# Optimization experiments

Measured on AMD Instinct MI355X. Metric: run time of the kernel, lower is better.

Reference implementation:

```python
import jax, jax.numpy as jnp
import numpy as np

B, LQ, LKV = 2, 2048, 2048
DQ, DKV, HID, NH = 1024, 1024, 1024, 16
HD = HID // NH
EPS = 1e-5


def setup_inputs() -> dict:
    key = jax.random.key(0)
    ks = jax.random.split(key, 12)
    s_q = 1.0 / np.sqrt(DQ)
    s_kv = 1.0 / np.sqrt(DKV)
    s_h = 1.0 / np.sqrt(HID)
    return {
        "query": jax.random.normal(ks[0], (B, LQ, DQ), jnp.float32),
        "key_value": jax.random.normal(ks[1], (B, LKV, DKV), jnp.float32),
        "Wq": jax.random.uniform(ks[2], (DQ, HID), jnp.float32, -s_q, s_q),
        "bq": jax.random.uniform(ks[3], (HID,), jnp.float32, -s_q, s_q),
        "Wk": jax.random.uniform(ks[4], (DKV, HID), jnp.float32, -s_kv, s_kv),
        "bk": jax.random.uniform(ks[5], (HID,), jnp.float32, -s_kv, s_kv),
        "Wv": jax.random.uniform(ks[6], (DKV, HID), jnp.float32, -s_kv, s_kv),
        "bv": jax.random.uniform(ks[7], (HID,), jnp.float32, -s_kv, s_kv),
        "Wo": jax.random.uniform(ks[8], (HID, DQ), jnp.float32, -s_h, s_h),
        "bo": jax.random.uniform(ks[9], (DQ,), jnp.float32, -s_h, s_h),
        "ln_gamma": jnp.ones((DQ,), jnp.float32),
        "ln_beta": jnp.zeros((DQ,), jnp.float32),
    }


def reference(query, key_value, Wq, bq, Wk, bk, Wv, bv, Wo, bo, ln_gamma, ln_beta):
    b, lq, _ = query.shape
    lkv = key_value.shape[1]
    # projections -> [b, heads, len, head_dim]
    Q = (query @ Wq + bq).reshape(b, lq, NH, HD).transpose(0, 2, 1, 3)
    K = (key_value @ Wk + bk).reshape(b, lkv, NH, HD).transpose(0, 2, 1, 3)
    V = (key_value @ Wv + bv).reshape(b, lkv, NH, HD).transpose(0, 2, 1, 3)
    scores = jnp.einsum("bhqd,bhkd->bhqk", Q, K) / jnp.sqrt(jnp.float32(HD))
    attn = jax.nn.softmax(scores, axis=-1)
    ctx = jnp.einsum("bhqk,bhkd->bhqd", attn, V)
    ctx = ctx.transpose(0, 2, 1, 3).reshape(b, lq, HID)
    out = ctx @ Wo + bo
    x = query + out
    mu = jnp.mean(x, axis=-1, keepdims=True)
    var = jnp.mean(jnp.square(x - mu), axis=-1, keepdims=True)
    return (x - mu) / jnp.sqrt(var + EPS) * ln_gamma + ln_beta
```

## Files before the change

kernel.cpp:

```cpp
#include <hip/hip_runtime.h>

typedef unsigned short u16;
typedef __bf16 bf16x8 __attribute__((ext_vector_type(8)));
typedef float f32x4 __attribute__((ext_vector_type(4)));
typedef unsigned short u16x4 __attribute__((ext_vector_type(4)));

#define LOG2E 1.44269504088896340736f
#define LDK 1040
#define LDV 2080
#define EXPM16 12599160.0f

__device__ __forceinline__ u16 f2bf(float f) {
  unsigned u = __float_as_uint(f);
  u += 0x7FFFu + ((u >> 16) & 1u);
  return (u16)(u >> 16);
}

__device__ __forceinline__ void load_lds16(const void* g, void* l) {
  __builtin_amdgcn_global_load_lds(
      (__attribute__((address_space(1))) void*)g,
      (__attribute__((address_space(3))) void*)l, 16, 0, 0);
}

__device__ __forceinline__ f32x4 mfma16(bf16x8 a, bf16x8 b, f32x4 c) {
  return __builtin_amdgcn_mfma_f32_16x16x32_bf16(a, b, c, 0, 0, 0);
}

__global__ __launch_bounds__(256) void pre_kernel(
    const float* __restrict__ q, const float* __restrict__ kv,
    u16* __restrict__ Xq, u16* __restrict__ Xkv,
    const float* __restrict__ Wq, const float* __restrict__ Wk,
    const float* __restrict__ Wv, const float* __restrict__ Wo,
    u16* __restrict__ Wqt, u16* __restrict__ Wkt,
    u16* __restrict__ Wvt, u16* __restrict__ Wot) {
  __shared__ float tile[32][33];
  const int bid = blockIdx.x;
  if (bid < 8192) {
    const int n4each = 4096 * 256;
    int i = bid * 256 + threadIdx.x;
    const float* src; u16* dst; int j;
    if (i < n4each) { src = q; dst = Xq; j = i; }
    else            { src = kv; dst = Xkv; j = i - n4each; }
    const float4 v = ((const float4*)src)[j];
    u16x4 o;
    o.x = f2bf(v.x); o.y = f2bf(v.y); o.z = f2bf(v.z); o.w = f2bf(v.w);
    ((u16x4*)dst)[j] = o;
    return;
  }
  const int t = bid - 8192;
  const int z = t >> 10, rem = t & 1023;
  const float* W; u16* Wt;
  switch (z) {
    case 0: W = Wq; Wt = Wqt; break;
    case 1: W = Wk; Wt = Wkt; break;
    case 2: W = Wv; Wt = Wvt; break;
    default: W = Wo; Wt = Wot; break;
  }
  const int tx = threadIdx.x & 31, ty = threadIdx.x >> 5;
  const int n0 = (rem & 31) * 32, k0 = (rem >> 5) * 32;
#pragma unroll
  for (int i = 0; i < 4; i++)
    tile[ty + i * 8][tx] = W[(size_t)(k0 + ty + i * 8) * 1024 + n0 + tx];
  __syncthreads();
#pragma unroll
  for (int i = 0; i < 4; i++)
    Wt[(size_t)(n0 + ty + i * 8) * 1024 + k0 + tx] = f2bf(tile[tx][ty + i * 8]);
}

__device__ __forceinline__ void gemm_tile(
    const u16* __restrict__ A, int lda, const u16* __restrict__ Bt, int ldb,
    const float* __restrict__ bias, bool brow, float scale,
    u16* __restrict__ Cb, float* __restrict__ Cf,
    int ldc, int bm, int bn, int K) {
  __shared__ alignas(16) u16 As[128 * 32];
  __shared__ alignas(16) u16 Bs[128 * 32];
  const int tid = threadIdx.x;
  const int wave = tid >> 6, lane = tid & 63;
  const int lm = lane & 15, kq = lane >> 4;
  const int g1 = tid, g2 = tid + 256;
  const u16* Ag1 = A + (size_t)(bm + (g1 >> 2)) * lda + (g1 & 3) * 8;
  const u16* Ag2 = A + (size_t)(bm + (g2 >> 2)) * lda + (g2 & 3) * 8;
  const u16* Bg1 = Bt + (size_t)(bn + (g1 >> 2)) * ldb + (g1 & 3) * 8;
  const u16* Bg2 = Bt + (size_t)(bn + (g2 >> 2)) * ldb + (g2 & 3) * 8;
  u16* lA1 = &As[g1 * 8]; u16* lA2 = &As[g2 * 8];
  u16* lB1 = &Bs[g1 * 8]; u16* lB2 = &Bs[g2 * 8];
  const int wm = (wave >> 1) * 64, wn = (wave & 1) * 64;

  f32x4 acc[4][4] = {};
  for (int k0 = 0; k0 < K; k0 += 32) {
    __syncthreads();
    load_lds16(Ag1 + k0, lA1);
    load_lds16(Ag2 + k0, lA2);
    load_lds16(Bg1 + k0, lB1);
    load_lds16(Bg2 + k0, lB2);
    __syncthreads();
    bf16x8 a[4], b[4];
#pragma unroll
    for (int t = 0; t < 4; t++)
      a[t] = *(const bf16x8*)&As[(wm + t * 16 + lm) * 32 + kq * 8];
#pragma unroll
    for (int t = 0; t < 4; t++)
      b[t] = *(const bf16x8*)&Bs[(wn + t * 16 + lm) * 32 + kq * 8];
#pragma unroll
    for (int mt = 0; mt < 4; mt++)
#pragma unroll
      for (int nt = 0; nt < 4; nt++)
        acc[mt][nt] = mfma16(a[mt], b[nt], acc[mt][nt]);
  }
#pragma unroll
  for (int mt = 0; mt < 4; mt++) {
    float rb[4];
#pragma unroll
    for (int r = 0; r < 4; r++)
      rb[r] = (bias && brow) ? bias[bm + wm + mt * 16 + kq * 4 + r] : 0.f;
#pragma unroll
    for (int nt = 0; nt < 4; nt++) {
      const int col = bn + wn + nt * 16 + lm;
      const float cb = (bias && !brow) ? bias[col] : 0.f;
#pragma unroll
      for (int r = 0; r < 4; r++) {
        const int row = bm + wm + mt * 16 + kq * 4 + r;
        const size_t idx = (size_t)row * ldc + col;
        const float v = (acc[mt][nt][r] + rb[r] + cb) * scale;
        if (Cf) Cf[idx] = v;
        else    Cb[idx] = f2bf(v);
      }
    }
  }
}

__global__ __launch_bounds__(256) void proj_gemm_kernel(
    const u16* __restrict__ Xq, const u16* __restrict__ Xkv,
    const u16* __restrict__ Wqt, const u16* __restrict__ Wkt, const u16* __restrict__ Wvt,
    const float* __restrict__ bq, const float* __restrict__ bk, const float* __restrict__ bv,
    u16* __restrict__ Qp, u16* __restrict__ Kp, u16* __restrict__ Vt, float qscale) {
  const int bid = blockIdx.x;
  const u16 *A, *Bt; const float* bias; u16* C;
  bool brow = false; float sc = 1.f; int ldc = 1024; int bm, bn;
  if (bid < 512) {
    const int r = bid & 255;
    const int xcd = r & 7, s = r >> 3;
    bm = (xcd * 4 + (s >> 3)) * 128;
    bn = (s & 7) * 128;
    if (bid < 256) { A = Xq;  Bt = Wqt; bias = bq; C = Qp; sc = qscale; }
    else           { A = Xkv; Bt = Wkt; bias = bk; C = Kp; ldc = LDK;  }
  } else {
    int r = bid - 512;
    const int z = r >> 7; r &= 127;
    const int xcd = r & 7, s = r >> 3;
    bm = (s >> 1) * 128;
    bn = (xcd * 2 + (s & 1)) * 128;
    A = Wvt; Bt = Xkv + (size_t)z * 2048 * 1024; bias = bv; brow = true;
    C = Vt + (size_t)z * 1024 * LDV; ldc = LDV;
  }
  gemm_tile(A, 1024, Bt, 1024, bias, brow, sc, C, nullptr, ldc, bm, bn, 1024);
}

__global__ __launch_bounds__(256) void ogemm_kernel(
    const u16* __restrict__ Ctx, const u16* __restrict__ Wot,
    float* __restrict__ X0, float* __restrict__ X1) {
  const int z = blockIdx.z;
  float* Cf = z ? X1 : X0;
  const int lin = blockIdx.x + 8 * blockIdx.y;
  const int xcd = lin & 7, s = lin >> 3;
  const int bm = (xcd * 4 + (s >> 3)) * 128, bn = (s & 7) * 128;
  gemm_tile(Ctx + z * 512, 1024, Wot + z * 512, 1024, nullptr, false, 1.f,
            nullptr, Cf, 1024, bm, bn, 512);
}

__global__ __launch_bounds__(256) void attn_kernel(
    const u16* __restrict__ Qp, const u16* __restrict__ Kp,
    const u16* __restrict__ Vt, u16* __restrict__ ctx) {
  __shared__ alignas(16) u16 Ks[2 * 4096];
  __shared__ alignas(16) u16 Vs[2 * 4096];
  const int tid = threadIdx.x;
  const int wave = tid >> 6, lane = tid & 63;
  const int lm = lane & 15, kq = lane >> 4;
  const int L = blockIdx.x;
  const int xcd = L & 7, s = L >> 3;
  const int combo = xcd + 8 * (s >> 4);
  const int qb = s & 15;
  const int h = combo & 15, b = combo >> 4;
  const int qbase = qb * 128 + wave * 32;

  bf16x8 qf[2][2];
#pragma unroll
  for (int qt = 0; qt < 2; qt++)
#pragma unroll
    for (int kc = 0; kc < 2; kc++)
      qf[qt][kc] = *(const bf16x8*)(Qp + (size_t)(b * 2048 + qbase + qt * 16 + lm) * 1024 +
                                    h * 64 + kc * 32 + kq * 8);

  union { u16 u[8]; bf16x8 v; } uo;
#pragma unroll
  for (int i = 0; i < 8; i++) uo.u[i] = 0x3F80;
  const bf16x8 ones = uo.v;

  const u16* Kb = Kp + (size_t)(b * 2048) * LDK + h * 64;
  const u16* Vb = Vt + (size_t)(b * 1024 + h * 64) * LDV;
  const int sp = lane ^ ((lane >> 3) & 7);
  const int c4 = sp >> 2, c3 = sp & 3;
  const int kvsw = ((lm * 4 + kq) ^ (lm >> 1)) * 8;

  f32x4 o[4][2] = {};
  f32x4 lsum[2] = {};

#pragma unroll
  for (int j = 0; j < 2; j++) {
    const int ii = wave * 2 + j;
    const u16* gk = Kb + (size_t)(16 * (ii & 3) + c4) * LDK + (ii >> 2) * 32 + c3 * 8;
    load_lds16(gk, &Ks[ii * 512 + lane * 8]);
    const u16* gv = Vb + (size_t)(16 * (ii & 3) + c4) * LDV + (ii >> 2) * 32 + c3 * 8;
    load_lds16(gv, &Vs[ii * 512 + lane * 8]);
  }

  int cur = 0;
  for (int t = 0; t < 32; ++t) {
    {
      const int kvn = ((t + 1) & 31) * 64;
      const int nb = (cur ^ 1) * 4096;
#pragma unroll
      for (int j = 0; j < 2; j++) {
        const int ii = wave * 2 + j;
        const u16* gk = Kb + (size_t)(kvn + 16 * (ii & 3) + c4) * LDK + (ii >> 2) * 32 + c3 * 8;
        load_lds16(gk, &Ks[nb + ii * 512 + lane * 8]);
        const u16* gv = Vb + (size_t)(16 * (ii & 3) + c4) * LDV + kvn + (ii >> 2) * 32 + c3 * 8;
        load_lds16(gv, &Vs[nb + ii * 512 + lane * 8]);
      }
    }
    __builtin_amdgcn_sched_barrier(0);
    asm volatile("s_waitcnt vmcnt(4)" ::: "memory");
    __builtin_amdgcn_sched_barrier(0);
    __builtin_amdgcn_s_barrier();

    const int cb = cur * 4096;
    __builtin_amdgcn_s_setprio(1);

    bf16x8 kf[2][4];
#pragma unroll
    for (int kc = 0; kc < 2; kc++)
#pragma unroll
      for (int kvt = 0; kvt < 4; kvt++)
        kf[kc][kvt] = *(const bf16x8*)&Ks[cb + kc * 2048 + kvt * 512 + kvsw];

    bf16x8 pf[2][2];
#pragma unroll
    for (int qt = 0; qt < 2; qt++) {
      f32x4 st[4] = {};
#pragma unroll
      for (int kc = 0; kc < 2; kc++)
#pragma unroll
        for (int kvt = 0; kvt < 4; kvt++)
          st[kvt] = mfma16(kf[kc][kvt], qf[qt][kc], st[kvt]);
      unsigned Xd[4][2];
#pragma unroll
      for (int kvt = 0; kvt < 4; kvt++) {
        const unsigned e0 = __float_as_uint(fmaf(st[kvt][0], 128.f, EXPM16));
        const unsigned e1 = __float_as_uint(fmaf(st[kvt][1], 128.f, EXPM16));
        const unsigned e2 = __float_as_uint(fmaf(st[kvt][2], 128.f, EXPM16));
        const unsigned e3 = __float_as_uint(fmaf(st[kvt][3], 128.f, EXPM16));
        Xd[kvt][0] = __builtin_amdgcn_perm(e1, e0, 0x05040100u);
        Xd[kvt][1] = __builtin_amdgcn_perm(e3, e2, 0x05040100u);
      }
#pragma unroll
      for (int K1 = 0; K1 < 2; K1++) {
        unsigned a0 = Xd[2 * K1][0], b0 = Xd[2 * K1 + 1][0];
        unsigned a1 = Xd[2 * K1][1], b1 = Xd[2 * K1 + 1][1];
        asm("v_permlane32_swap_b32 %0, %1\n\t"
            "v_permlane16_swap_b32 %0, %1"
            : "+v"(a0), "+v"(b0));
        asm("v_permlane32_swap_b32 %0, %1\n\t"
            "v_permlane16_swap_b32 %0, %1"
            : "+v"(a1), "+v"(b1));
        union { uint4 u; bf16x8 v; } c;
        c.u.x = a0; c.u.y = a1; c.u.z = b0; c.u.w = b1;
        pf[qt][K1] = c.v;
      }
    }
#pragma unroll
    for (int s2 = 0; s2 < 2; s2++) {
      bf16x8 vf[4];
#pragma unroll
      for (int hdt = 0; hdt < 4; hdt++)
        vf[hdt] = *(const bf16x8*)&Vs[cb + s2 * 2048 + hdt * 512 + kvsw];
#pragma unroll
      for (int qt = 0; qt < 2; qt++) {
        lsum[qt] = mfma16(ones, pf[qt][s2], lsum[qt]);
#pragma unroll
        for (int hdt = 0; hdt < 4; hdt++)
          o[hdt][qt] = mfma16(vf[hdt], pf[qt][s2], o[hdt][qt]);
      }
    }
    __builtin_amdgcn_s_setprio(0);
    __builtin_amdgcn_sched_barrier(0);
    __builtin_amdgcn_s_barrier();
    cur ^= 1;
  }
#pragma unroll
  for (int qt = 0; qt < 2; qt++) {
    const float rl = 1.f / lsum[qt][0];
    u16* cbp = ctx + (size_t)(b * 2048 + qbase + qt * 16 + lm) * 1024 + h * 64 + kq * 4;
#pragma unroll
    for (int hdt = 0; hdt < 4; hdt++) {
      u16x4 w;
#pragma unroll
      for (int r = 0; r < 4; r++) w[r] = f2bf(o[hdt][qt][r] * rl);
      *(u16x4*)(cbp + hdt * 16) = w;
    }
  }
}

__global__ __launch_bounds__(256) void ln_kernel(
    const float* __restrict__ x0, const float* __restrict__ x1,
    const float* __restrict__ q, const float* __restrict__ bo,
    const float* __restrict__ gamma, const float* __restrict__ beta,
    float* __restrict__ out) {
  const int row = blockIdx.x;
  const int t = threadIdx.x;
  const size_t g = (size_t)row * 256 + t;
  const float4 a = ((const float4*)x0)[g];
  const float4 c = ((const float4*)x1)[g];
  const float4 d = ((const float4*)q)[g];
  const float4 bv = ((const float4*)bo)[t];
  float4 v;
  v.x = a.x + c.x + d.x + bv.x;
  v.y = a.y + c.y + d.y + bv.y;
  v.z = a.z + c.z + d.z + bv.z;
  v.w = a.w + c.w + d.w + bv.w;
  float s = v.x + v.y + v.z + v.w;
  float s2 = v.x * v.x + v.y * v.y + v.z * v.z + v.w * v.w;
#pragma unroll
  for (int m = 1; m < 64; m <<= 1) {
    s += __shfl_xor(s, m);
    s2 += __shfl_xor(s2, m);
  }
  __shared__ float red[8];
  const int wave = t >> 6, lane = t & 63;
  if (lane == 0) { red[wave] = s; red[4 + wave] = s2; }
  __syncthreads();
  s = red[0] + red[1] + red[2] + red[3];
  s2 = red[4] + red[5] + red[6] + red[7];
  const float mu = s * (1.f / 1024.f);
  const float var = s2 * (1.f / 1024.f) - mu * mu;
  const float rstd = rsqrtf(var + 1e-5f);
  const float4 gm = ((const float4*)gamma)[t];
  const float4 bt = ((const float4*)beta)[t];
  float4 o;
  o.x = (v.x - mu) * rstd * gm.x + bt.x;
  o.y = (v.y - mu) * rstd * gm.y + bt.y;
  o.z = (v.z - mu) * rstd * gm.z + bt.z;
  o.w = (v.w - mu) * rstd * gm.w + bt.w;
  ((float4*)(out + (size_t)row * 1024))[t] = o;
}

extern "C" void kernel_launch(void* const* d_in, const int* in_sizes, int n_in,
                              void* d_out, int out_size, void* d_ws, size_t ws_size,
                              hipStream_t stream) {
  const float* query     = (const float*)d_in[0];
  const float* key_value = (const float*)d_in[1];
  const float* Wq = (const float*)d_in[2];
  const float* bq = (const float*)d_in[3];
  const float* Wk = (const float*)d_in[4];
  const float* bk = (const float*)d_in[5];
  const float* Wv = (const float*)d_in[6];
  const float* bv = (const float*)d_in[7];
  const float* Wo = (const float*)d_in[8];
  const float* bo = (const float*)d_in[9];
  const float* gamma = (const float*)d_in[10];
  const float* beta  = (const float*)d_in[11];
  float* out = (float*)d_out;

  const size_t MT = (size_t)4096 * 1024;
  const size_t WT = (size_t)1024 * 1024;
  char* ws = (char*)d_ws;
  u16* Xq  = (u16*)ws; ws += MT * 2;
  u16* Xkv = (u16*)ws; ws += MT * 2;
  u16* Wqt = (u16*)ws; ws += WT * 2;
  u16* Wkt = (u16*)ws; ws += WT * 2;
  u16* Wvt = (u16*)ws; ws += WT * 2;
  u16* Wot = (u16*)ws; ws += WT * 2;
  u16* Qp  = (u16*)ws; ws += MT * 2;
  u16* Kp  = (u16*)ws; ws += (size_t)4096 * LDK * 2;
  u16* Vt  = (u16*)ws; ws += (size_t)2048 * LDV * 2;
  float* X0 = (float*)ws; ws += MT * 4;
  float* X1 = (float*)ws; ws += MT * 4;
  u16* Ctx = Xq;

  const float qscale = 0.125f * LOG2E;

  pre_kernel<<<12288, 256, 0, stream>>>(query, key_value, Xq, Xkv,
                                        Wq, Wk, Wv, Wo, Wqt, Wkt, Wvt, Wot);
  proj_gemm_kernel<<<768, 256, 0, stream>>>(Xq, Xkv, Wqt, Wkt, Wvt, bq, bk, bv,
                                            Qp, Kp, Vt, qscale);
  attn_kernel<<<512, 256, 0, stream>>>(Qp, Kp, Vt, Ctx);
  ogemm_kernel<<<dim3(8, 32, 2), 256, 0, stream>>>(Ctx, Wot, X0, X1);
  ln_kernel<<<4096, 256, 0, stream>>>(X0, X1, query, bo, gamma, beta, out);
}
```

Baseline: 213.5 us.

## Split attention KV range across two wave groups and merge partial outputs in LDS

The attention block grows from 4 to 8 waves. Each half processes half of the KV sequence (1024 keys) over 16 iterations instead of 32, with separate double-buffered K/V LDS regions. At the end, the second half writes its partial O and row sums to shared memory and the first half combines them and writes ctx. This works without max-rescaling because the softmax uses a fixed-offset exp trick. The aim is to halve the serial KV loop length and raise parallelism per block, at the cost of more LDS (64KB), an extra reduction step, and possibly lower occupancy.

```diff
diff --git a/kernel.cpp b/kernel.cpp
--- a/kernel.cpp
+++ b/kernel.cpp
@@ -168,20 +168,23 @@
             nullptr, Cf, 1024, bm, bn, 512);
 }
 
-__global__ __launch_bounds__(256) void attn_kernel(
+__global__ __launch_bounds__(512, 4) void attn_kernel(
     const u16* __restrict__ Qp, const u16* __restrict__ Kp,
     const u16* __restrict__ Vt, u16* __restrict__ ctx) {
-  __shared__ alignas(16) u16 Ks[2 * 4096];
-  __shared__ alignas(16) u16 Vs[2 * 4096];
+  __shared__ alignas(16) u16 smem[32768];
   const int tid = threadIdx.x;
   const int wave = tid >> 6, lane = tid & 63;
+  const int kh = wave >> 2, w4 = wave & 3;
   const int lm = lane & 15, kq = lane >> 4;
   const int L = blockIdx.x;
   const int xcd = L & 7, s = L >> 3;
   const int combo = xcd + 8 * (s >> 4);
   const int qb = s & 15;
   const int h = combo & 15, b = combo >> 4;
-  const int qbase = qb * 128 + wave * 32;
+  const int qbase = qb * 128 + w4 * 32;
+
+  u16* Ksh = smem + kh * 8192;
+  u16* Vsh = smem + 16384 + kh * 8192;
 
   bf16x8 qf[2][2];
 #pragma unroll
@@ -196,8 +199,8 @@
   for (int i = 0; i < 8; i++) uo.u[i] = 0x3F80;
   const bf16x8 ones = uo.v;
 
-  const u16* Kb = Kp + (size_t)(b * 2048) * LDK + h * 64;
-  const u16* Vb = Vt + (size_t)(b * 1024 + h * 64) * LDV;
+  const u16* Kb = Kp + ((size_t)b * 2048 + kh * 1024) * LDK + h * 64;
+  const u16* Vb = Vt + (size_t)(b * 1024 + h * 64) * LDV + kh * 1024;
   const int sp = lane ^ ((lane >> 3) & 7);
   const int c4 = sp >> 2, c3 = sp & 3;
   const int kvsw = ((lm * 4 + kq) ^ (lm >> 1)) * 8;
@@ -207,30 +210,33 @@
 
 #pragma unroll
   for (int j = 0; j < 2; j++) {
-    const int ii = wave * 2 + j;
+    const int ii = w4 * 2 + j;
     const u16* gk = Kb + (size_t)(16 * (ii & 3) + c4) * LDK + (ii >> 2) * 32 + c3 * 8;
-    load_lds16(gk, &Ks[ii * 512 + lane * 8]);
+    load_lds16(gk, &Ksh[ii * 512 + lane * 8]);
     const u16* gv = Vb + (size_t)(16 * (ii & 3) + c4) * LDV + (ii >> 2) * 32 + c3 * 8;
-    load_lds16(gv, &Vs[ii * 512 + lane * 8]);
+    load_lds16(gv, &Vsh[ii * 512 + lane * 8]);
   }
 
   int cur = 0;
-  for (int t = 0; t < 32; ++t) {
-    {
-      const int kvn = ((t + 1) & 31) * 64;
+  for (int t = 0; t < 16; ++t) {
+    if (t < 15) {
+      const int kvn = (t + 1) * 64;
       const int nb = (cur ^ 1) * 4096;
 #pragma unroll
       for (int j = 0; j < 2; j++) {
-        const int ii = wave * 2 + j;
+        const int ii = w4 * 2 + j;
         const u16* gk = Kb + (size_t)(kvn + 16 * (ii & 3) + c4) * LDK + (ii >> 2) * 32 + c3 * 8;
-        load_lds16(gk, &Ks[nb + ii * 512 + lane * 8]);
+        load_lds16(gk, &Ksh[nb + ii * 512 + lane * 8]);
         const u16* gv = Vb + (size_t)(16 * (ii & 3) + c4) * LDV + kvn + (ii >> 2) * 32 + c3 * 8;
-        load_lds16(gv, &Vs[nb + ii * 512 + lane * 8]);
-      }
+        load_lds16(gv, &Vsh[nb + ii * 512 + lane * 8]);
+      }
+      __builtin_amdgcn_sched_barrier(0);
+      asm volatile("s_waitcnt vmcnt(4)" ::: "memory");
+    } else {
+      __builtin_amdgcn_sched_barrier(0);
+      asm volatile("s_waitcnt vmcnt(0)" ::: "memory");
     }
     __builtin_amdgcn_sched_barrier(0);
-    asm volatile("s_waitcnt vmcnt(4)" ::: "memory");
-    __builtin_amdgcn_sched_barrier(0);
     __builtin_amdgcn_s_barrier();
 
     const int cb = cur * 4096;
@@ -241,7 +247,7 @@
     for (int kc = 0; kc < 2; kc++)
 #pragma unroll
       for (int kvt = 0; kvt < 4; kvt++)
-        kf[kc][kvt] = *(const bf16x8*)&Ks[cb + kc * 2048 + kvt * 512 + kvsw];
+        kf[kc][kvt] = *(const bf16x8*)&Ksh[cb + kc * 2048 + kvt * 512 + kvsw];
 
     bf16x8 pf[2][2];
 #pragma unroll
@@ -282,7 +288,7 @@
       bf16x8 vf[4];
 #pragma unroll
       for (int hdt = 0; hdt < 4; hdt++)
-        vf[hdt] = *(const bf16x8*)&Vs[cb + s2 * 2048 + hdt * 512 + kvsw];
+        vf[hdt] = *(const bf16x8*)&Vsh[cb + s2 * 2048 + hdt * 512 + kvsw];
 #pragma unroll
       for (int qt = 0; qt < 2; qt++) {
         lsum[qt] = mfma16(ones, pf[qt][s2], lsum[qt]);
@@ -296,16 +302,34 @@
     __builtin_amdgcn_s_barrier();
     cur ^= 1;
   }
-#pragma unroll
-  for (int qt = 0; qt < 2; qt++) {
-    const float rl = 1.f / lsum[qt][0];
-    u16* cbp = ctx + (size_t)(b * 2048 + qbase + qt * 16 + lm) * 1024 + h * 64 + kq * 4;
-#pragma unroll
-    for (int hdt = 0; hdt < 4; hdt++) {
-      u16x4 w;
-#pragma unroll
-      for (int r = 0; r < 4; r++) w[r] = f2bf(o[hdt][qt][r] * rl);
-      *(u16x4*)(cbp + hdt * 16) = w;
+
+  __syncthreads();
+  float* ex = (float*)smem;
+  const int exi = (w4 * 64 + lane) * 36;
+  if (kh == 1) {
+#pragma unroll
+    for (int qt = 0; qt < 2; qt++)
+#pragma unroll
+      for (int hdt = 0; hdt < 4; hdt++)
+        *(f32x4*)&ex[exi + (qt * 4 + hdt) * 4] = o[hdt][qt];
+    ex[exi + 32] = lsum[0][0];
+    ex[exi + 33] = lsum[1][0];
+  }
+  __syncthreads();
+  if (kh == 0) {
+#pragma unroll
+    for (int qt = 0; qt < 2; qt++) {
+      const float lo = ex[exi + 32 + qt];
+      const float rl = 1.f / (lsum[qt][0] + lo);
+      u16* cbp = ctx + (size_t)(b * 2048 + qbase + qt * 16 + lm) * 1024 + h * 64 + kq * 4;
+#pragma unroll
+      for (int hdt = 0; hdt < 4; hdt++) {
+        const f32x4 op = *(const f32x4*)&ex[exi + (qt * 4 + hdt) * 4];
+        u16x4 w;
+#pragma unroll
+        for (int r = 0; r < 4; r++) w[r] = f2bf((o[hdt][qt][r] + op[r]) * rl);
+        *(u16x4*)(cbp + hdt * 16) = w;
+      }
     }
   }
 }
@@ -392,7 +416,7 @@
                                         Wq, Wk, Wv, Wo, Wqt, Wkt, Wvt, Wot);
   proj_gemm_kernel<<<768, 256, 0, stream>>>(Xq, Xkv, Wqt, Wkt, Wvt, bq, bk, bv,
                                             Qp, Kp, Vt, qscale);
-  attn_kernel<<<512, 256, 0, stream>>>(Qp, Kp, Vt, Ctx);
+  attn_kernel<<<512, 512, 0, stream>>>(Qp, Kp, Vt, Ctx);
   ogemm_kernel<<<dim3(8, 32, 2), 256, 0, stream>>>(Ctx, Wot, X0, X1);
   ln_kernel<<<4096, 256, 0, stream>>>(X0, X1, query, bo, gamma, beta, out);
 }
```

After: 215.5 us, median of 2. No clear change (+0.9%).

## Use 8 waves per attention block with one 16-row query tile each

Applied to the files above, without the earlier changes.

The attention kernel now runs 512 threads (8 waves) per block instead of 4, and each wave handles 16 query rows instead of 32. Each wave loads one K/V chunk per iteration, and the final iteration skips the wrapped-around prefetch and waits with vmcnt(0). The aim is more waves for latency hiding and fewer registers per wave, at the cost of each K/V LDS fragment being reused by fewer MFMAs per wave and more barrier participants.

```diff
diff --git a/kernel.cpp b/kernel.cpp
--- a/kernel.cpp
+++ b/kernel.cpp
@@ -168,7 +168,7 @@
             nullptr, Cf, 1024, bm, bn, 512);
 }
 
-__global__ __launch_bounds__(256) void attn_kernel(
+__global__ __launch_bounds__(512, 6) void attn_kernel(
     const u16* __restrict__ Qp, const u16* __restrict__ Kp,
     const u16* __restrict__ Vt, u16* __restrict__ ctx) {
   __shared__ alignas(16) u16 Ks[2 * 4096];
@@ -181,15 +181,13 @@
   const int combo = xcd + 8 * (s >> 4);
   const int qb = s & 15;
   const int h = combo & 15, b = combo >> 4;
-  const int qbase = qb * 128 + wave * 32;
-
-  bf16x8 qf[2][2];
-#pragma unroll
-  for (int qt = 0; qt < 2; qt++)
-#pragma unroll
-    for (int kc = 0; kc < 2; kc++)
-      qf[qt][kc] = *(const bf16x8*)(Qp + (size_t)(b * 2048 + qbase + qt * 16 + lm) * 1024 +
-                                    h * 64 + kc * 32 + kq * 8);
+  const int qbase = qb * 128 + wave * 16;
+
+  bf16x8 qf[2];
+#pragma unroll
+  for (int kc = 0; kc < 2; kc++)
+    qf[kc] = *(const bf16x8*)(Qp + (size_t)(b * 2048 + qbase + lm) * 1024 +
+                              h * 64 + kc * 32 + kq * 8);
 
   union { u16 u[8]; bf16x8 v; } uo;
 #pragma unroll
@@ -202,34 +200,31 @@
   const int c4 = sp >> 2, c3 = sp & 3;
   const int kvsw = ((lm * 4 + kq) ^ (lm >> 1)) * 8;
 
-  f32x4 o[4][2] = {};
-  f32x4 lsum[2] = {};
-
-#pragma unroll
-  for (int j = 0; j < 2; j++) {
-    const int ii = wave * 2 + j;
-    const u16* gk = Kb + (size_t)(16 * (ii & 3) + c4) * LDK + (ii >> 2) * 32 + c3 * 8;
-    load_lds16(gk, &Ks[ii * 512 + lane * 8]);
-    const u16* gv = Vb + (size_t)(16 * (ii & 3) + c4) * LDV + (ii >> 2) * 32 + c3 * 8;
-    load_lds16(gv, &Vs[ii * 512 + lane * 8]);
+  f32x4 o[4] = {};
+  f32x4 lsum = {};
+
+  {
+    const u16* gk = Kb + (size_t)(16 * (wave & 3) + c4) * LDK + (wave >> 2) * 32 + c3 * 8;
+    load_lds16(gk, &Ks[wave * 512 + lane * 8]);
+    const u16* gv = Vb + (size_t)(16 * (wave & 3) + c4) * LDV + (wave >> 2) * 32 + c3 * 8;
+    load_lds16(gv, &Vs[wave * 512 + lane * 8]);
   }
 
   int cur = 0;
   for (int t = 0; t < 32; ++t) {
-    {
-      const int kvn = ((t + 1) & 31) * 64;
+    if (t < 31) {
+      const int kvn = (t + 1) * 64;
       const int nb = (cur ^ 1) * 4096;
-#pragma unroll
-      for (int j = 0; j < 2; j++) {
-        const int ii = wave * 2 + j;
-        const u16* gk = Kb + (size_t)(kvn + 16 * (ii & 3) + c4) * LDK + (ii >> 2) * 32 + c3 * 8;
-        load_lds16(gk, &Ks[nb + ii * 512 + lane * 8]);
-        const u16* gv = Vb + (size_t)(16 * (ii & 3) + c4) * LDV + kvn + (ii >> 2) * 32 + c3 * 8;
-        load_lds16(gv, &Vs[nb + ii * 512 + lane * 8]);
-      }
-    }
-    __builtin_amdgcn_sched_barrier(0);
-    asm volatile("s_waitcnt vmcnt(4)" ::: "memory");
+      const u16* gk = Kb + (size_t)(kvn + 16 * (wave & 3) + c4) * LDK + (wave >> 2) * 32 + c3 * 8;
+      load_lds16(gk, &Ks[nb + wave * 512 + lane * 8]);
+      const u16* gv = Vb + (size_t)(16 * (wave & 3) + c4) * LDV + kvn + (wave >> 2) * 32 + c3 * 8;
+      load_lds16(gv, &Vs[nb + wave * 512 + lane * 8]);
+      __builtin_amdgcn_sched_barrier(0);
+      asm volatile("s_waitcnt vmcnt(2)" ::: "memory");
+    } else {
+      __builtin_amdgcn_sched_barrier(0);
+      asm volatile("s_waitcnt vmcnt(0)" ::: "memory");
+    }
     __builtin_amdgcn_sched_barrier(0);
     __builtin_amdgcn_s_barrier();
 
@@ -243,39 +238,37 @@
       for (int kvt = 0; kvt < 4; kvt++)
         kf[kc][kvt] = *(const bf16x8*)&Ks[cb + kc * 2048 + kvt * 512 + kvsw];
 
-    bf16x8 pf[2][2];
-#pragma unroll
-    for (int qt = 0; qt < 2; qt++) {
-      f32x4 st[4] = {};
-#pragma unroll
-      for (int kc = 0; kc < 2; kc++)
-#pragma unroll
-        for (int kvt = 0; kvt < 4; kvt++)
-          st[kvt] = mfma16(kf[kc][kvt], qf[qt][kc], st[kvt]);
-      unsigned Xd[4][2];
-#pragma unroll
-      for (int kvt = 0; kvt < 4; kvt++) {
-        const unsigned e0 = __float_as_uint(fmaf(st[kvt][0], 128.f, EXPM16));
-        const unsigned e1 = __float_as_uint(fmaf(st[kvt][1], 128.f, EXPM16));
-        const unsigned e2 = __float_as_uint(fmaf(st[kvt][2], 128.f, EXPM16));
-        const unsigned e3 = __float_as_uint(fmaf(st[kvt][3], 128.f, EXPM16));
-        Xd[kvt][0] = __builtin_amdgcn_perm(e1, e0, 0x05040100u);
-        Xd[kvt][1] = __builtin_amdgcn_perm(e3, e2, 0x05040100u);
-      }
-#pragma unroll
-      for (int K1 = 0; K1 < 2; K1++) {
-        unsigned a0 = Xd[2 * K1][0], b0 = Xd[2 * K1 + 1][0];
-        unsigned a1 = Xd[2 * K1][1], b1 = Xd[2 * K1 + 1][1];
-        asm("v_permlane32_swap_b32 %0, %1\n\t"
-            "v_permlane16_swap_b32 %0, %1"
-            : "+v"(a0), "+v"(b0));
-        asm("v_permlane32_swap_b32 %0, %1\n\t"
-            "v_permlane16_swap_b32 %0, %1"
-            : "+v"(a1), "+v"(b1));
-        union { uint4 u; bf16x8 v; } c;
-        c.u.x = a0; c.u.y = a1; c.u.z = b0; c.u.w = b1;
-        pf[qt][K1] = c.v;
-      }
+    f32x4 st[4] = {};
+#pragma unroll
+    for (int kc = 0; kc < 2; kc++)
+#pragma unroll
+      for (int kvt = 0; kvt < 4; kvt++)
+        st[kvt] = mfma16(kf[kc][kvt], qf[kc], st[kvt]);
+
+    unsigned Xd[4][2];
+#pragma unroll
+    for (int kvt = 0; kvt < 4; kvt++) {
+      const unsigned e0 = __float_as_uint(fmaf(st[kvt][0], 128.f, EXPM16));
+      const unsigned e1 = __float_as_uint(fmaf(st[kvt][1], 128.f, EXPM16));
+      const unsigned e2 = __float_as_uint(fmaf(st[kvt][2], 128.f, EXPM16));
+      const unsigned e3 = __float_as_uint(fmaf(st[kvt][3], 128.f, EXPM16));
+      Xd[kvt][0] = __builtin_amdgcn_perm(e1, e0, 0x05040100u);
+      Xd[kvt][1] = __builtin_amdgcn_perm(e3, e2, 0x05040100u);
+    }
+    bf16x8 pf[2];
+#pragma unroll
+    for (int K1 = 0; K1 < 2; K1++) {
+      unsigned a0 = Xd[2 * K1][0], b0 = Xd[2 * K1 + 1][0];
+      unsigned a1 = Xd[2 * K1][1], b1 = Xd[2 * K1 + 1][1];
+      asm("v_permlane32_swap_b32 %0, %1\n\t"
+          "v_permlane16_swap_b32 %0, %1"
+          : "+v"(a0), "+v"(b0));
+      asm("v_permlane32_swap_b32 %0, %1\n\t"
+          "v_permlane16_swap_b32 %0, %1"
+          : "+v"(a1), "+v"(b1));
+      union { uint4 u; bf16x8 v; } c;
+      c.u.x = a0; c.u.y = a1; c.u.z = b0; c.u.w = b1;
+      pf[K1] = c.v;
     }
 #pragma unroll
     for (int s2 = 0; s2 < 2; s2++) {
@@ -283,30 +276,25 @@
 #pragma unroll
       for (int hdt = 0; hdt < 4; hdt++)
         vf[hdt] = *(const bf16x8*)&Vs[cb + s2 * 2048 + hdt * 512 + kvsw];
-#pragma unroll
-      for (int qt = 0; qt < 2; qt++) {
-        lsum[qt] = mfma16(ones, pf[qt][s2], lsum[qt]);
-#pragma unroll
-        for (int hdt = 0; hdt < 4; hdt++)
-          o[hdt][qt] = mfma16(vf[hdt], pf[qt][s2], o[hdt][qt]);
-      }
+      lsum = mfma16(ones, pf[s2], lsum);
+#pragma unroll
+      for (int hdt = 0; hdt < 4; hdt++)
+        o[hdt] = mfma16(vf[hdt], pf[s2], o[hdt]);
     }
     __builtin_amdgcn_s_setprio(0);
     __builtin_amdgcn_sched_barrier(0);
     __builtin_amdgcn_s_barrier();
     cur ^= 1;
   }
-#pragma unroll
-  for (int qt = 0; qt < 2; qt++) {
-    const float rl = 1.f / lsum[qt][0];
-    u16* cbp = ctx + (size_t)(b * 2048 + qbase + qt * 16 + lm) * 1024 + h * 64 + kq * 4;
-#pragma unroll
-    for (int hdt = 0; hdt < 4; hdt++) {
-      u16x4 w;
-#pragma unroll
-      for (int r = 0; r < 4; r++) w[r] = f2bf(o[hdt][qt][r] * rl);
-      *(u16x4*)(cbp + hdt * 16) = w;
-    }
+
+  const float rl = 1.f / lsum[0];
+  u16* cbp = ctx + (size_t)(b * 2048 + qbase + lm) * 1024 + h * 64 + kq * 4;
+#pragma unroll
+  for (int hdt = 0; hdt < 4; hdt++) {
+    u16x4 w;
+#pragma unroll
+    for (int r = 0; r < 4; r++) w[r] = f2bf(o[hdt][r] * rl);
+    *(u16x4*)(cbp + hdt * 16) = w;
   }
 }
 
@@ -392,7 +380,7 @@
                                         Wq, Wk, Wv, Wo, Wqt, Wkt, Wvt, Wot);
   proj_gemm_kernel<<<768, 256, 0, stream>>>(Xq, Xkv, Wqt, Wkt, Wvt, bq, bk, bv,
                                             Qp, Kp, Vt, qscale);
-  attn_kernel<<<512, 256, 0, stream>>>(Qp, Kp, Vt, Ctx);
+  attn_kernel<<<512, 512, 0, stream>>>(Qp, Kp, Vt, Ctx);
   ogemm_kernel<<<dim3(8, 32, 2), 256, 0, stream>>>(Ctx, Wot, X0, X1);
   ln_kernel<<<4096, 256, 0, stream>>>(X0, X1, query, bo, gamma, beta, out);
 }
```

New measurement: 210.3 us. No clear change (-1.5%).
